# Kernel optimization log

Measured on AMD Instinct MI355X. Metric: run time of the kernel, lower is better.

## Reference

```python
import jax, jax.numpy as jnp
import numpy as np

RHO = 1.0  # Lorentz curvature parameter


def setup_inputs() -> dict:
    key = jax.random.key(0)
    k1, k2, k3 = jax.random.split(key, 3)
    C, S, n, d = 512, 256, 16, 8  # cells, sites, states, hyperbolic dim
    # points on the Lorentz hyperboloid <x,x>_L = -RHO
    v = jax.random.normal(k1, (C, d), jnp.float32) * 0.5
    x0 = jnp.sqrt(RHO + jnp.sum(v * v, axis=-1, keepdims=True))
    X = jnp.concatenate([x0, v], axis=-1)  # [C, d+1]
    # per-site CTMC rate matrices: nonneg off-diagonal, rows sum to 0
    R = jax.random.uniform(k2, (S, n, n), jnp.float32) * 0.1
    R = R * (1.0 - jnp.eye(n, dtype=jnp.float32))
    Q = R - jnp.eye(n, dtype=jnp.float32) * jnp.sum(R, axis=-1)[..., None]
    char = jax.random.randint(k3, (C, S), 0, n).astype(jnp.int32)
    return {"X": X, "Q": Q, "char": char, "i": 0}


def _gather_last(A, idx):
    # A: [..., n], idx: [...] int -> A[..., idx] elementwise
    return jnp.take_along_axis(A, idx[..., None], axis=-1)[..., 0]


def reference(X, Q, char, i):
    C, S = char.shape
    n = Q.shape[-1]
    xi = X[i]
    # Lorentz (Minkowski) inner product and geodesic distance
    inner = -xi[0] * X[:, 0] + X[:, 1:] @ xi[1:]            # [C]
    u = jnp.maximum(-inner / RHO, 1.0 + 1e-6)
    dist = jnp.sqrt(RHO) * jnp.arccosh(u)                    # [C]
    t = 0.5 * dist
    # per-(cell j, site) transition probabilities P = expm(t_j * Q_site)
    M = t[:, None, None, None] * Q[None]                     # [C,S,n,n]
    P = jax.vmap(jax.scipy.linalg.expm)(M.reshape(-1, n, n)).reshape(C, S, n, n)
    s_i = char[i]                                            # [S]
    s_j = char                                               # [C,S]
    si_b = jnp.broadcast_to(s_i[None, :], (C, S))
    # ancestor a = 0 (unedited root state) is always feasible
    P0 = P[:, :, 0, :]                                       # [C,S,n]
    p0_si = _gather_last(P0, si_b)
    p0_sj = _gather_last(P0, s_j)
    # ancestor a = s is feasible iff s_i == s_j == s != 0 (irreversible edits)
    row_idx = jnp.broadcast_to(si_b[:, :, None, None], (C, S, 1, n))
    Prow = jnp.take_along_axis(P, row_idx, axis=2)[:, :, 0, :]  # P[c,s,s_i,:]
    ps_si = _gather_last(Prow, si_b)
    ps_sj = _gather_last(Prow, s_j)
    same = (si_b == s_j) & (si_b != 0)
    pi = 1.0 / n  # uniform stationary distribution
    cur = pi * (p0_si * p0_sj + jnp.where(same, ps_si * ps_sj, 0.0))  # [C,S]
    valid = jnp.arange(C) != i
    ll = jnp.where(valid[:, None], jnp.log(cur), 0.0)
    return jnp.sum(ll)
```

## Files before the change

### kernel.cpp

```cpp
#include <hip/hip_runtime.h>
#include <math.h>

#define C_N 512
#define S_N 256
#define NN  16
#define DP1 9
#define KT  16
#define KTP 20

__global__ __launch_bounds__(256) void site_kernel(
    const float* __restrict__ X, const float* __restrict__ Q,
    const int* __restrict__ ch, const int* __restrict__ ip,
    float* __restrict__ partials)
{
    const int s   = blockIdx.x;
    const int tid = threadIdx.x;
    const int wid = tid >> 6;

    __shared__ __align__(16) float w0T[NN][KTP];
    __shared__ __align__(16) float w1T[NN][KTP];
    __shared__ float lam_sh;
    __shared__ float red[4];

    const float* __restrict__ Qs = Q + s * NN * NN;
    const int i0 = ip[0];
    const int si = ch[i0 * S_N + s];

    if (wid < 2) {
        const int lane = tid & 63;
        const int j = lane & 15;
        const int q = lane >> 4;
        float dmax = -Qs[j * NN + j];
        #pragma unroll
        for (int off = 1; off < 16; off <<= 1)
            dmax = fmaxf(dmax, __shfl_xor(dmax, off, 64));
        const float lam = dmax;
        if (tid == 0) lam_sh = lam;
        const float rl = 1.0f / lam;

        float a[4];
        #pragma unroll
        for (int m = 0; m < 4; ++m) {
            const int r = 4 * q + m;
            a[m] = Qs[r * NN + j] * rl + (r == j ? 1.0f : 0.0f);
        }

        float (*WT)[KTP] = (wid == 0) ? w0T : w1T;
        const int tgt = (wid == 0) ? 0 : si;
        float w = (j == tgt) ? 1.0f : 0.0f;
        if (q == 0) WT[j][0] = w;

        #pragma unroll
        for (int k = 1; k < KT; ++k) {
            float acc = 0.0f;
            #pragma unroll
            for (int m = 0; m < 4; ++m)
                acc = fmaf(__shfl(w, 4 * q + m, 64), a[m], acc);
            acc += __shfl_xor(acc, 16, 64);
            acc += __shfl_xor(acc, 32, 64);
            w = acc;
            if (q == 0) WT[j][k] = w;
        }
    }

    const float* __restrict__ xi = X + i0 * DP1;
    const float x0i = xi[0];
    float vi[8];
    #pragma unroll
    for (int d = 0; d < 8; ++d) vi[d] = xi[1 + d];

    float x_c[2]; int sj_c[2]; bool ok_c[2];
    #pragma unroll
    for (int cc = 0; cc < 2; ++cc) {
        const int c = tid + cc * 256;
        ok_c[cc] = (c != i0);
        const float* __restrict__ xc = X + c * DP1;
        float inner = -x0i * xc[0];
        #pragma unroll
        for (int d = 0; d < 8; ++d) inner = fmaf(vi[d], xc[1 + d], inner);
        const float u = fmaxf(-inner, 1.0f + 1e-6f);
        const float dist = __logf(u + __fsqrt_rn(fmaf(u, u, -1.0f)));
        x_c[cc]  = 0.5f * dist;
        sj_c[cc] = ch[c * S_N + s];
    }
    __syncthreads();
    const float lam = lam_sh;

    float partial = 0.0f;
    #pragma unroll
    for (int cc = 0; cc < 2; ++cc) {
        const float x  = lam * x_c[cc];
        const int   sj = sj_c[cc];
        const float4* __restrict__ u0p = (const float4*)&w0T[si][0];
        const float4* __restrict__ u1p = (const float4*)&w0T[sj][0];
        const float4* __restrict__ u2p = (const float4*)&w1T[si][0];
        const float4* __restrict__ u3p = (const float4*)&w1T[sj][0];
        float p = __expf(-x);
        float a0 = 0.f, a1 = 0.f, a2 = 0.f, a3 = 0.f;
        #pragma unroll
        for (int kb = 0; kb < 4; ++kb) {
            const float4 f0 = u0p[kb], f1 = u1p[kb], f2 = u2p[kb], f3 = u3p[kb];
            #define STEP(K, CMP)                                   \
                a0 = fmaf(p, f0.CMP, a0);                          \
                a1 = fmaf(p, f1.CMP, a1);                          \
                a2 = fmaf(p, f2.CMP, a2);                          \
                a3 = fmaf(p, f3.CMP, a3);                          \
                p *= x * (1.0f / (float)((K) + 1));
            STEP(4 * kb + 0, x)
            STEP(4 * kb + 1, y)
            STEP(4 * kb + 2, z)
            STEP(4 * kb + 3, w)
            #undef STEP
        }
        const bool same = (si == sj) && (si != 0);
        const float cur = 0.0625f * (a0 * a1 + (same ? a2 * a3 : 0.0f));
        if (ok_c[cc]) partial += __logf(cur);
    }

    #pragma unroll
    for (int off = 32; off; off >>= 1)
        partial += __shfl_down(partial, off, 64);
    if ((tid & 63) == 0) red[tid >> 6] = partial;
    __syncthreads();
    if (tid == 0) partials[s] = red[0] + red[1] + red[2] + red[3];
}

__global__ __launch_bounds__(256) void reduce_kernel(
    const float* __restrict__ partials, float* __restrict__ out)
{
    const int tid = threadIdx.x;
    __shared__ float red[4];
    float v = partials[tid];
    #pragma unroll
    for (int off = 32; off; off >>= 1)
        v += __shfl_down(v, off, 64);
    if ((tid & 63) == 0) red[tid >> 6] = v;
    __syncthreads();
    if (tid == 0) out[0] = red[0] + red[1] + red[2] + red[3];
}

extern "C" void kernel_launch(void* const* d_in, const int* in_sizes, int n_in,
                              void* d_out, int out_size, void* d_ws, size_t ws_size,
                              hipStream_t stream) {
    const float* X  = (const float*)d_in[0];
    const float* Q  = (const float*)d_in[1];
    const int*   ch = (const int*)d_in[2];
    const int*   ip = (const int*)d_in[3];
    float* out      = (float*)d_out;
    float* partials = (float*)d_ws;

    site_kernel<<<S_N, 256, 0, stream>>>(X, Q, ch, ip, partials);
    reduce_kernel<<<1, 256, 0, stream>>>(partials, out);
}
```

Measured before the change: 11.90 us.

## Use one thread per cell and Horner-evaluate factorial-scaled uniformization series

Folds the 1/k! factors into the shared-memory uniformization coefficients and evaluates each series with a Horner recurrence in x. The exp(-x) factor is pulled out and applied in log space as -2x, which drops the per-cell exp and the running product. The block grows to 512 threads so each thread handles one cell instead of two, adding parallelism per site. Risks include float underflow in the small high-order coefficients and higher register pressure from keeping all coefficients in registers.

```diff
diff --git a/kernel.cpp b/kernel.cpp
--- a/kernel.cpp
+++ b/kernel.cpp
@@ -8,7 +8,7 @@
 #define KT  16
 #define KTP 20
 
-__global__ __launch_bounds__(256) void site_kernel(
+__global__ __launch_bounds__(512) void site_kernel(
     const float* __restrict__ X, const float* __restrict__ Q,
     const int* __restrict__ ch, const int* __restrict__ ip,
     float* __restrict__ partials)
@@ -17,10 +17,10 @@
     const int tid = threadIdx.x;
     const int wid = tid >> 6;
 
-    __shared__ __align__(16) float w0T[NN][KTP];
-    __shared__ __align__(16) float w1T[NN][KTP];
+    __shared__ __align__(16) float wh0T[NN][KTP];
+    __shared__ __align__(16) float wh1T[NN][KTP];
     __shared__ float lam_sh;
-    __shared__ float red[4];
+    __shared__ float red[8];
 
     const float* __restrict__ Qs = Q + s * NN * NN;
     const int i0 = ip[0];
@@ -45,7 +45,13 @@
             a[m] = Qs[r * NN + j] * rl + (r == j ? 1.0f : 0.0f);
         }
 
-        float (*WT)[KTP] = (wid == 0) ? w0T : w1T;
+        constexpr float IF[KT] = {
+            1.f, 1.f, 5.0e-1f, 1.6666667e-1f, 4.1666667e-2f, 8.3333333e-3f,
+            1.3888889e-3f, 1.9841270e-4f, 2.4801587e-5f, 2.7557319e-6f,
+            2.7557319e-7f, 2.5052108e-8f, 2.0876757e-9f, 1.6059044e-10f,
+            1.1470746e-11f, 7.6471637e-13f };
+
+        float (*WT)[KTP] = (wid == 0) ? wh0T : wh1T;
         const int tgt = (wid == 0) ? 0 : si;
         float w = (j == tgt) ? 1.0f : 0.0f;
         if (q == 0) WT[j][0] = w;
@@ -59,7 +65,7 @@
             acc += __shfl_xor(acc, 16, 64);
             acc += __shfl_xor(acc, 32, 64);
             w = acc;
-            if (q == 0) WT[j][k] = w;
+            if (q == 0) WT[j][k] = w * IF[k];
         }
     }
 
@@ -69,60 +75,59 @@
     #pragma unroll
     for (int d = 0; d < 8; ++d) vi[d] = xi[1 + d];
 
-    float x_c[2]; int sj_c[2]; bool ok_c[2];
+    const int c = tid;
+    const bool ok = (c != i0);
+    const float* __restrict__ xc = X + c * DP1;
+    float inner = -x0i * xc[0];
     #pragma unroll
-    for (int cc = 0; cc < 2; ++cc) {
-        const int c = tid + cc * 256;
-        ok_c[cc] = (c != i0);
-        const float* __restrict__ xc = X + c * DP1;
-        float inner = -x0i * xc[0];
-        #pragma unroll
-        for (int d = 0; d < 8; ++d) inner = fmaf(vi[d], xc[1 + d], inner);
-        const float u = fmaxf(-inner, 1.0f + 1e-6f);
-        const float dist = __logf(u + __fsqrt_rn(fmaf(u, u, -1.0f)));
-        x_c[cc]  = 0.5f * dist;
-        sj_c[cc] = ch[c * S_N + s];
-    }
+    for (int d = 0; d < 8; ++d) inner = fmaf(vi[d], xc[1 + d], inner);
+    const float u = fmaxf(-inner, 1.0f + 1e-6f);
+    const float dist = __logf(u + __fsqrt_rn(fmaf(u, u, -1.0f)));
+    const float thalf = 0.5f * dist;
+    const int sj = ch[c * S_N + s];
+
     __syncthreads();
-    const float lam = lam_sh;
+    const float x = lam_sh * thalf;
 
-    float partial = 0.0f;
-    #pragma unroll
-    for (int cc = 0; cc < 2; ++cc) {
-        const float x  = lam * x_c[cc];
-        const int   sj = sj_c[cc];
-        const float4* __restrict__ u0p = (const float4*)&w0T[si][0];
-        const float4* __restrict__ u1p = (const float4*)&w0T[sj][0];
-        const float4* __restrict__ u2p = (const float4*)&w1T[si][0];
-        const float4* __restrict__ u3p = (const float4*)&w1T[sj][0];
-        float p = __expf(-x);
-        float a0 = 0.f, a1 = 0.f, a2 = 0.f, a3 = 0.f;
+    float4 f0[4], f1[4], f2[4], f3[4];
+    {
+        const float4* __restrict__ u0p = (const float4*)&wh0T[si][0];
+        const float4* __restrict__ u1p = (const float4*)&wh0T[sj][0];
+        const float4* __restrict__ u2p = (const float4*)&wh1T[si][0];
+        const float4* __restrict__ u3p = (const float4*)&wh1T[sj][0];
         #pragma unroll
         for (int kb = 0; kb < 4; ++kb) {
-            const float4 f0 = u0p[kb], f1 = u1p[kb], f2 = u2p[kb], f3 = u3p[kb];
-            #define STEP(K, CMP)                                   \
-                a0 = fmaf(p, f0.CMP, a0);                          \
-                a1 = fmaf(p, f1.CMP, a1);                          \
-                a2 = fmaf(p, f2.CMP, a2);                          \
-                a3 = fmaf(p, f3.CMP, a3);                          \
-                p *= x * (1.0f / (float)((K) + 1));
-            STEP(4 * kb + 0, x)
-            STEP(4 * kb + 1, y)
-            STEP(4 * kb + 2, z)
-            STEP(4 * kb + 3, w)
-            #undef STEP
+            f0[kb] = u0p[kb]; f1[kb] = u1p[kb];
+            f2[kb] = u2p[kb]; f3[kb] = u3p[kb];
         }
-        const bool same = (si == sj) && (si != 0);
-        const float cur = 0.0625f * (a0 * a1 + (same ? a2 * a3 : 0.0f));
-        if (ok_c[cc]) partial += __logf(cur);
     }
+    const float* c0 = (const float*)f0;
+    const float* c1 = (const float*)f1;
+    const float* c2 = (const float*)f2;
+    const float* c3 = (const float*)f3;
+    float h0 = c0[KT - 1], h1 = c1[KT - 1], h2 = c2[KT - 1], h3 = c3[KT - 1];
+    #pragma unroll
+    for (int k = KT - 2; k >= 0; --k) {
+        h0 = fmaf(h0, x, c0[k]);
+        h1 = fmaf(h1, x, c1[k]);
+        h2 = fmaf(h2, x, c2[k]);
+        h3 = fmaf(h3, x, c3[k]);
+    }
+    const bool same = (si == sj) && (si != 0);
+    const float prod = h0 * h1 + (same ? h2 * h3 : 0.0f);
+    float partial = ok ? (__logf(0.0625f * prod) - 2.0f * x) : 0.0f;
 
     #pragma unroll
     for (int off = 32; off; off >>= 1)
         partial += __shfl_down(partial, off, 64);
-    if ((tid & 63) == 0) red[tid >> 6] = partial;
+    if ((tid & 63) == 0) red[wid] = partial;
     __syncthreads();
-    if (tid == 0) partials[s] = red[0] + red[1] + red[2] + red[3];
+    if (tid == 0) {
+        float acc = 0.0f;
+        #pragma unroll
+        for (int wv = 0; wv < 8; ++wv) acc += red[wv];
+        partials[s] = acc;
+    }
 }
 
 __global__ __launch_bounds__(256) void reduce_kernel(
@@ -149,6 +154,6 @@
     float* out      = (float*)d_out;
     float* partials = (float*)d_ws;
 
-    site_kernel<<<S_N, 256, 0, stream>>>(X, Q, ch, ip, partials);
+    site_kernel<<<S_N, 512, 0, stream>>>(X, Q, ch, ip, partials);
     reduce_kernel<<<1, 256, 0, stream>>>(partials, out);
 }
```

After: 11.83 us. Within noise of the previous version (-0.6%).
